# Performance work log

Hardware: AMD Instinct MI355X
Metric: run time of the kernel (lower is better)

Reference implementation:

```python
import jax, jax.numpy as jnp
import numpy as np

B, L, D = 4096, 200, 128


def setup_inputs() -> dict:
    key = jax.random.key(0)
    ks = jax.random.split(key, 9)
    s_in = 1.0 / np.sqrt(2 * D)  # torch Linear default init scale (uniform bound)
    inp = {
        "h_states": jax.random.normal(ks[0], (B, L, D), dtype=jnp.float32),
        "target_emb_proj": jax.random.normal(ks[1], (B, D), dtype=jnp.float32),
        "mask": jax.random.randint(ks[2], (B, L), 0, 2).astype(bool),
        "W_r": jax.random.uniform(ks[3], (2 * D, D), jnp.float32, -s_in, s_in),
        "b_r": jax.random.uniform(ks[4], (D,), jnp.float32, -s_in, s_in),
        "W_u": jax.random.uniform(ks[5], (2 * D, D), jnp.float32, -s_in, s_in),
        "b_u": jax.random.uniform(ks[6], (D,), jnp.float32, -s_in, s_in),
        "W_h": jax.random.uniform(ks[7], (2 * D, D), jnp.float32, -s_in, s_in),
        "b_h": jax.random.uniform(ks[8], (D,), jnp.float32, -s_in, s_in),
    }
    return inp


def reference(h_states, target_emb_proj, mask, W_r, b_r, W_u, b_u, W_h, b_h):
    Bd, Ld, Dd = h_states.shape
    # target-aware attention scores over history: (B, L)
    scores = jnp.einsum("bld,bd->bl", h_states, target_emb_proj) / np.sqrt(Dd).astype(h_states.dtype)
    scores = jnp.where(mask, scores, jnp.asarray(-1e9, scores.dtype))
    attn = jax.nn.softmax(scores, axis=-1)  # (B, L)

    xs = (
        jnp.transpose(h_states, (1, 0, 2)),  # (L, B, D)
        attn.T,                               # (L, B)
        mask.T,                               # (L, B)
    )

    def step(h, x):
        x_t, e_t, m_t = x
        combined = jnp.concatenate([x_t, h], axis=-1)  # (B, 2D)
        r = jax.nn.sigmoid(combined @ W_r + b_r)
        u = jax.nn.sigmoid(combined @ W_u + b_u)
        u_prime = e_t[:, None] * u
        h_tilde = jnp.tanh(jnp.concatenate([x_t, r * h], axis=-1) @ W_h + b_h)
        h_new = (1.0 - u_prime) * h + u_prime * h_tilde
        h_next = jnp.where(m_t[:, None], h_new, h)
        return h_next, None

    h0 = jnp.zeros((Bd, Dd), dtype=h_states.dtype)
    h_final, _ = jax.lax.scan(step, h0, xs)
    return h_final
```

## Files before the change

kernel.cpp:

```cpp
#include <hip/hip_runtime.h>
#include <hip/hip_bf16.h>
#include <stdint.h>

#define LSEQ 200
#define DDIM 128

typedef __attribute__((ext_vector_type(8))) __bf16 bf16x8;
typedef __attribute__((ext_vector_type(4))) float f32x4;

__device__ __forceinline__ float fast_exp(float x) {
  return __builtin_amdgcn_exp2f(x * 1.4426950408889634f);
}
__device__ __forceinline__ float fast_sigmoid(float x) {
  return __builtin_amdgcn_rcpf(1.0f + fast_exp(-x));
}
__device__ __forceinline__ float fast_tanh(float x) {
  float ax = __builtin_fabsf(x);
  float t = __builtin_amdgcn_exp2f(ax * -2.885390081777927f);
  float r = (1.0f - t) * __builtin_amdgcn_rcpf(1.0f + t);
  return x < 0.0f ? -r : r;
}

__device__ __forceinline__ f32x4 mfma16(bf16x8 a, bf16x8 b, f32x4 c) {
  return __builtin_amdgcn_mfma_f32_16x16x32_bf16(a, b, c, 0, 0, 0);
}

__global__ __launch_bounds__(512) void k_scores_pack(
    const float* __restrict__ h_states, const float* __restrict__ target,
    const int* __restrict__ mask, uint4* __restrict__ xp,
    float* __restrict__ attnT, int B) {
  __shared__ float s_sc[4][16][LSEQ];
  __shared__ float s_tgt[16][DDIM];
  const int b16 = blockIdx.x;
  const int bb = b16 * 16;
  const int tid = threadIdx.x;
  for (int i = tid; i < 16 * DDIM; i += 512)
    s_tgt[i >> 7][i & 127] = target[(size_t)(bb + (i >> 7)) * DDIM + (i & 127)];
  __syncthreads();

  const int lane = tid & 63;
  const int kt = (tid >> 6) & 3;
  const int tp = tid >> 8;
  const int row = lane & 15;
  const int hi = lane >> 4;
  const int kbase = kt * 32 + hi * 8;
  const int B16 = B >> 4;
  const float* src = h_states + ((size_t)(bb + row) * LSEQ) * DDIM + kbase;
  const float* tg = &s_tgt[row][kbase];

  for (int t = tp; t < LSEQ; t += 2) {
    float4 a = *(const float4*)(src + (size_t)t * DDIM);
    float4 b = *(const float4*)(src + (size_t)t * DDIM + 4);
    float dv = (a.x * tg[0] + a.y * tg[1] + a.z * tg[2] + a.w * tg[3]) +
               (b.x * tg[4] + b.y * tg[5] + b.z * tg[6] + b.w * tg[7]);
    dv += __shfl_xor(dv, 16);
    dv += __shfl_xor(dv, 32);
    if (hi == 0) s_sc[kt][row][t] = dv;
    union { __bf16 h[8]; uint4 v; } pk;
    pk.h[0] = (__bf16)a.x; pk.h[1] = (__bf16)a.y; pk.h[2] = (__bf16)a.z; pk.h[3] = (__bf16)a.w;
    pk.h[4] = (__bf16)b.x; pk.h[5] = (__bf16)b.y; pk.h[6] = (__bf16)b.z; pk.h[7] = (__bf16)b.w;
    xp[(((size_t)t * B16 + b16) * 4 + kt) * 64 + lane] = pk.v;
  }
  __syncthreads();

  if (tid < 256) {
    const int r2 = tid >> 4;
    const int j = tid & 15;
    const int* mrow = mask + (size_t)(bb + r2) * LSEQ;
    float mx = -3.0e38f;
    for (int t = j; t < LSEQ; t += 16) {
      float s = (s_sc[0][r2][t] + s_sc[1][r2][t]) + (s_sc[2][r2][t] + s_sc[3][r2][t]);
      s *= 0.088388347648318447f;
      s = (mrow[t] != 0) ? s : -3.0e38f;
      s_sc[0][r2][t] = s;
      mx = fmaxf(mx, s);
    }
    mx = fmaxf(mx, __shfl_xor(mx, 1));
    mx = fmaxf(mx, __shfl_xor(mx, 2));
    mx = fmaxf(mx, __shfl_xor(mx, 4));
    mx = fmaxf(mx, __shfl_xor(mx, 8));
    float se = 0.0f;
    for (int t = j; t < LSEQ; t += 16) {
      float e = fast_exp(s_sc[0][r2][t] - mx);
      s_sc[1][r2][t] = e;
      se += e;
    }
    se += __shfl_xor(se, 1);
    se += __shfl_xor(se, 2);
    se += __shfl_xor(se, 4);
    se += __shfl_xor(se, 8);
    float rs = __builtin_amdgcn_rcpf(se);
    for (int t = j; t < LSEQ; t += 16)
      attnT[(size_t)t * B + bb + r2] = (mrow[t] != 0) ? s_sc[1][r2][t] * rs : 0.0f;
  }
}

__global__ __launch_bounds__(512, 2) void k_recur(
    const uint4* __restrict__ xp, const float* __restrict__ attnT,
    const float* __restrict__ Wr, const float* __restrict__ br,
    const float* __restrict__ Wu, const float* __restrict__ bu,
    const float* __restrict__ Wh, const float* __restrict__ bh,
    float* __restrict__ out, int B) {
  __shared__ __bf16 s_rh[16][136];
  __shared__ __bf16 s_hb[16][136];
  __shared__ float s_att[LSEQ][16];
  const int tid = threadIdx.x;
  const int lane = tid & 63;
  const int wv = tid >> 6;
  const int b16 = blockIdx.x;
  const int bb = b16 * 16;
  const int g = lane >> 4;
  const int rA = lane & 15;
  const int col = wv * 16 + rA;
  const int B16 = B >> 4;

  bf16x8 wr[8], wu[8], wh[8];
#pragma unroll
  for (int kt = 0; kt < 8; ++kt) {
    bf16x8 tr, tu, th;
    int krow = kt * 32 + g * 8;
#pragma unroll
    for (int j = 0; j < 8; ++j) {
      tr[j] = (__bf16)Wr[(size_t)(krow + j) * DDIM + col];
      tu[j] = (__bf16)Wu[(size_t)(krow + j) * DDIM + col];
      th[j] = (__bf16)Wh[(size_t)(krow + j) * DDIM + col];
    }
    wr[kt] = tr; wu[kt] = tu; wh[kt] = th;
  }
  const float biasr = br[col], biasu = bu[col], biash = bh[col];

  for (int i = tid; i < LSEQ * 16; i += 512)
    s_att[i >> 4][i & 15] = attnT[(size_t)(i >> 4) * B + bb + (i & 15)];
  for (int i = tid; i < 16 * 136; i += 512)
    (&s_hb[0][0])[i] = (__bf16)0.0f;
  __syncthreads();

  float hD[4] = {0.f, 0.f, 0.f, 0.f};
  uint4 xc[4], xn[4];
  {
    size_t base = (size_t)b16 * 4;
#pragma unroll
    for (int kt = 0; kt < 4; ++kt) xc[kt] = xp[(base + kt) * 64 + lane];
  }

  for (int t = 0; t < LSEQ; ++t) {
    if (t + 1 < LSEQ) {
      size_t base = ((size_t)(t + 1) * B16 + b16) * 4;
#pragma unroll
      for (int kt = 0; kt < 4; ++kt) xn[kt] = xp[(base + kt) * 64 + lane];
    }
    bf16x8 hf[4];
#pragma unroll
    for (int kt = 0; kt < 4; ++kt)
      hf[kt] = *(const bf16x8*)&s_hb[rA][kt * 32 + g * 8];
    f32x4 accr = {biasr, biasr, biasr, biasr};
    f32x4 accu = {biasu, biasu, biasu, biasu};
#pragma unroll
    for (int kt = 0; kt < 4; ++kt) {
      bf16x8 a = __builtin_bit_cast(bf16x8, xc[kt]);
      accr = mfma16(a, wr[kt], accr);
      accu = mfma16(a, wu[kt], accu);
    }
#pragma unroll
    for (int kt = 0; kt < 4; ++kt) {
      accr = mfma16(hf[kt], wr[4 + kt], accr);
      accu = mfma16(hf[kt], wu[4 + kt], accu);
    }
    float rr[4], uu[4];
#pragma unroll
    for (int j = 0; j < 4; ++j) {
      rr[j] = fast_sigmoid(accr[j]);
      uu[j] = fast_sigmoid(accu[j]);
      s_rh[g * 4 + j][col] = (__bf16)(rr[j] * hD[j]);
    }
    __builtin_amdgcn_sched_barrier(0);
    asm volatile("s_waitcnt lgkmcnt(0)" ::: "memory");
    __builtin_amdgcn_s_barrier();
    __builtin_amdgcn_sched_barrier(0);
    bf16x8 rf[4];
#pragma unroll
    for (int kt = 0; kt < 4; ++kt)
      rf[kt] = *(const bf16x8*)&s_rh[rA][kt * 32 + g * 8];
    f32x4 acch = {biash, biash, biash, biash};
#pragma unroll
    for (int kt = 0; kt < 4; ++kt) {
      bf16x8 a = __builtin_bit_cast(bf16x8, xc[kt]);
      acch = mfma16(a, wh[kt], acch);
      acch = mfma16(rf[kt], wh[4 + kt], acch);
    }
#pragma unroll
    for (int j = 0; j < 4; ++j) {
      float ht = fast_tanh(acch[j]);
      float up = s_att[t][g * 4 + j] * uu[j];
      hD[j] += up * (ht - hD[j]);
      s_hb[g * 4 + j][col] = (__bf16)hD[j];
    }
    __builtin_amdgcn_sched_barrier(0);
    asm volatile("s_waitcnt lgkmcnt(0)" ::: "memory");
    __builtin_amdgcn_s_barrier();
    __builtin_amdgcn_sched_barrier(0);
#pragma unroll
    for (int kt = 0; kt < 4; ++kt) xc[kt] = xn[kt];
  }
#pragma unroll
  for (int j = 0; j < 4; ++j)
    out[(size_t)(bb + g * 4 + j) * DDIM + col] = hD[j];
}

extern "C" void kernel_launch(void* const* d_in, const int* in_sizes, int n_in,
                              void* d_out, int out_size, void* d_ws, size_t ws_size,
                              hipStream_t stream) {
  const float* h_states = (const float*)d_in[0];
  const float* target   = (const float*)d_in[1];
  const int*   mask     = (const int*)d_in[2];
  const float* Wr = (const float*)d_in[3];
  const float* br = (const float*)d_in[4];
  const float* Wu = (const float*)d_in[5];
  const float* bu = (const float*)d_in[6];
  const float* Wh = (const float*)d_in[7];
  const float* bh = (const float*)d_in[8];

  const int B = in_sizes[0] / (LSEQ * DDIM);
  uint4* xp = (uint4*)d_ws;
  float* attnT = (float*)((char*)d_ws + (size_t)B * LSEQ * DDIM * 2);

  k_scores_pack<<<B / 16, 512, 0, stream>>>(h_states, target, mask, xp, attnT, B);
  k_recur<<<B / 16, 512, 0, stream>>>(xp, attnT, Wr, br, Wu, bu, Wh, bh,
                                      (float*)d_out, B);
}
```

Before: 316.8 us.

## Fuse score/pack kernel into recurrence and precompute next-step input projections

Merges the scoring/softmax/bf16-pack kernel with the GRU recurrence kernel into one launch per 16-row batch tile. The attention weights now stay in shared memory instead of going through a global buffer, and the packed x layout becomes batch-major so each block reads its own contiguous region. The recurrence is software-pipelined: the x-projection MFMAs for step t+1 are issued during step t, off the h-dependent critical path, with a two-step unrolled loop. This raises shared memory and register use per block, which can reduce occupancy, and it removes the overlap that separate kernels had between the bandwidth-heavy pack phase and compute.

```diff
diff --git a/kernel.cpp b/kernel.cpp
--- a/kernel.cpp
+++ b/kernel.cpp
@@ -25,43 +25,128 @@
   return __builtin_amdgcn_mfma_f32_16x16x32_bf16(a, b, c, 0, 0, 0);
 }
 
-__global__ __launch_bounds__(512) void k_scores_pack(
+#define STEP(t, XC, XN, AXRC, AXUC, AXHC, AXRN, AXUN, AXHN)             \
+  do {                                                                  \
+    if ((t) + 2 < LSEQ) {                                               \
+      size_t pbase = ((size_t)b16 * LSEQ + (t) + 2) * 4;                \
+      _Pragma("unroll") for (int kt = 0; kt < 4; ++kt)                  \
+          XN[kt] = xp[(pbase + kt) * 64 + lane];                        \
+    }                                                                   \
+    bf16x8 hf[4];                                                       \
+    _Pragma("unroll") for (int kt = 0; kt < 4; ++kt)                    \
+        hf[kt] = *(const bf16x8*)&s_hb[rA][kt * 32 + g * 8];            \
+    f32x4 accr = AXRC, accu = AXUC;                                     \
+    if ((t) + 1 < LSEQ) {   \
+      AXRN = (f32x4){biasr, biasr, biasr, biasr};                       \
+      AXUN = (f32x4){biasu, biasu, biasu, biasu};                       \
+      _Pragma("unroll") for (int kt = 0; kt < 4; ++kt) {                \
+        bf16x8 a = __builtin_bit_cast(bf16x8, XC[kt]);                  \
+        AXRN = mfma16(a, wr[kt], AXRN);                                 \
+        AXUN = mfma16(a, wu[kt], AXUN);                                 \
+      }                                                                 \
+    }                                                                   \
+    _Pragma("unroll") for (int kt = 0; kt < 4; ++kt) {                  \
+      accr = mfma16(hf[kt], wr[4 + kt], accr);                          \
+      accu = mfma16(hf[kt], wu[4 + kt], accu);                          \
+    }                                                                   \
+    float rr[4], uu[4];                                                 \
+    _Pragma("unroll") for (int j = 0; j < 4; ++j) {                     \
+      rr[j] = fast_sigmoid(accr[j]);                                    \
+      uu[j] = fast_sigmoid(accu[j]);                                    \
+      s_rh[g * 4 + j][col] = (__bf16)(rr[j] * hD[j]);                   \
+    }                                                                   \
+    __builtin_amdgcn_sched_barrier(0);                                  \
+    asm volatile("s_waitcnt lgkmcnt(0)" ::: "memory");                  \
+    __builtin_amdgcn_s_barrier();                                       \
+    __builtin_amdgcn_sched_barrier(0);                                  \
+    bf16x8 rf[4];                                                       \
+    _Pragma("unroll") for (int kt = 0; kt < 4; ++kt)                    \
+        rf[kt] = *(const bf16x8*)&s_rh[rA][kt * 32 + g * 8];            \
+    f32x4 acch = AXHC;                                                  \
+    if ((t) + 1 < LSEQ) {                                               \
+      AXHN = (f32x4){biash, biash, biash, biash};                       \
+      _Pragma("unroll") for (int kt = 0; kt < 4; ++kt)                  \
+        AXHN = mfma16(__builtin_bit_cast(bf16x8, XC[kt]), wh[kt], AXHN);\
+    }                                                                   \
+    _Pragma("unroll") for (int kt = 0; kt < 4; ++kt)                    \
+      acch = mfma16(rf[kt], wh[4 + kt], acch);                          \
+    _Pragma("unroll") for (int j = 0; j < 4; ++j) {                     \
+      float ht = fast_tanh(acch[j]);                                    \
+      float up = s_att[t][g * 4 + j] * uu[j];                           \
+      hD[j] += up * (ht - hD[j]);                                       \
+      s_hb[g * 4 + j][col] = (__bf16)hD[j];                             \
+    }                                                                   \
+    __builtin_amdgcn_sched_barrier(0);                                  \
+    asm volatile("s_waitcnt lgkmcnt(0)" ::: "memory");                  \
+    __builtin_amdgcn_s_barrier();                                       \
+    __builtin_amdgcn_sched_barrier(0);                                  \
+  } while (0)
+
+__global__ __launch_bounds__(512, 2) void k_fused(
     const float* __restrict__ h_states, const float* __restrict__ target,
-    const int* __restrict__ mask, uint4* __restrict__ xp,
-    float* __restrict__ attnT, int B) {
+    const int* __restrict__ mask,
+    const float* __restrict__ Wr, const float* __restrict__ br,
+    const float* __restrict__ Wu, const float* __restrict__ bu,
+    const float* __restrict__ Wh, const float* __restrict__ bh,
+    uint4* __restrict__ xp, float* __restrict__ out, int B) {
   __shared__ float s_sc[4][16][LSEQ];
   __shared__ float s_tgt[16][DDIM];
+  __shared__ float s_att[LSEQ][16];
+  __shared__ __bf16 s_rh[16][136];
+  __shared__ __bf16 s_hb[16][136];
+
   const int b16 = blockIdx.x;
   const int bb = b16 * 16;
   const int tid = threadIdx.x;
+  const int lane = tid & 63;
+  const int wv = tid >> 6;
+
   for (int i = tid; i < 16 * DDIM; i += 512)
     s_tgt[i >> 7][i & 127] = target[(size_t)(bb + (i >> 7)) * DDIM + (i & 127)];
   __syncthreads();
 
-  const int lane = tid & 63;
-  const int kt = (tid >> 6) & 3;
-  const int tp = tid >> 8;
-  const int row = lane & 15;
-  const int hi = lane >> 4;
-  const int kbase = kt * 32 + hi * 8;
-  const int B16 = B >> 4;
-  const float* src = h_states + ((size_t)(bb + row) * LSEQ) * DDIM + kbase;
-  const float* tg = &s_tgt[row][kbase];
-
-  for (int t = tp; t < LSEQ; t += 2) {
-    float4 a = *(const float4*)(src + (size_t)t * DDIM);
-    float4 b = *(const float4*)(src + (size_t)t * DDIM + 4);
-    float dv = (a.x * tg[0] + a.y * tg[1] + a.z * tg[2] + a.w * tg[3]) +
-               (b.x * tg[4] + b.y * tg[5] + b.z * tg[6] + b.w * tg[7]);
-    dv += __shfl_xor(dv, 16);
-    dv += __shfl_xor(dv, 32);
-    if (hi == 0) s_sc[kt][row][t] = dv;
-    union { __bf16 h[8]; uint4 v; } pk;
-    pk.h[0] = (__bf16)a.x; pk.h[1] = (__bf16)a.y; pk.h[2] = (__bf16)a.z; pk.h[3] = (__bf16)a.w;
-    pk.h[4] = (__bf16)b.x; pk.h[5] = (__bf16)b.y; pk.h[6] = (__bf16)b.z; pk.h[7] = (__bf16)b.w;
-    xp[(((size_t)t * B16 + b16) * 4 + kt) * 64 + lane] = pk.v;
+  {
+    const int kt = (tid >> 6) & 3;
+    const int tp = tid >> 8;
+    const int row = lane & 15;
+    const int hi = lane >> 4;
+    const int kbase = kt * 32 + hi * 8;
+    const float* src = h_states + ((size_t)(bb + row) * LSEQ) * DDIM + kbase;
+    const float* tg = &s_tgt[row][kbase];
+#pragma unroll 2
+    for (int t = tp; t < LSEQ; t += 2) {
+      float4 a = *(const float4*)(src + (size_t)t * DDIM);
+      float4 b = *(const float4*)(src + (size_t)t * DDIM + 4);
+      float dv = (a.x * tg[0] + a.y * tg[1] + a.z * tg[2] + a.w * tg[3]) +
+                 (b.x * tg[4] + b.y * tg[5] + b.z * tg[6] + b.w * tg[7]);
+      dv += __shfl_xor(dv, 16);
+      dv += __shfl_xor(dv, 32);
+      if (hi == 0) s_sc[kt][row][t] = dv;
+      union { __bf16 h[8]; uint4 v; } pk;
+      pk.h[0] = (__bf16)a.x; pk.h[1] = (__bf16)a.y; pk.h[2] = (__bf16)a.z; pk.h[3] = (__bf16)a.w;
+      pk.h[4] = (__bf16)b.x; pk.h[5] = (__bf16)b.y; pk.h[6] = (__bf16)b.z; pk.h[7] = (__bf16)b.w;
+      xp[(((size_t)b16 * LSEQ + t) * 4 + kt) * 64 + lane] = pk.v;
+    }
   }
   __syncthreads();
+
+  const int g = lane >> 4;
+  const int rA = lane & 15;
+  const int col = wv * 16 + rA;
+  bf16x8 wr[8], wu[8], wh[8];
+#pragma unroll
+  for (int kt = 0; kt < 8; ++kt) {
+    bf16x8 tr, tu, th;
+    int krow = kt * 32 + g * 8;
+#pragma unroll
+    for (int j = 0; j < 8; ++j) {
+      tr[j] = (__bf16)Wr[(size_t)(krow + j) * DDIM + col];
+      tu[j] = (__bf16)Wu[(size_t)(krow + j) * DDIM + col];
+      th[j] = (__bf16)Wh[(size_t)(krow + j) * DDIM + col];
+    }
+    wr[kt] = tr; wu[kt] = tu; wh[kt] = th;
+  }
+  const float biasr = br[col], biasu = bu[col], biash = bh[col];
 
   if (tid < 256) {
     const int r2 = tid >> 4;
@@ -91,117 +176,38 @@
     se += __shfl_xor(se, 8);
     float rs = __builtin_amdgcn_rcpf(se);
     for (int t = j; t < LSEQ; t += 16)
-      attnT[(size_t)t * B + bb + r2] = (mrow[t] != 0) ? s_sc[1][r2][t] * rs : 0.0f;
-  }
-}
-
-__global__ __launch_bounds__(512, 2) void k_recur(
-    const uint4* __restrict__ xp, const float* __restrict__ attnT,
-    const float* __restrict__ Wr, const float* __restrict__ br,
-    const float* __restrict__ Wu, const float* __restrict__ bu,
-    const float* __restrict__ Wh, const float* __restrict__ bh,
-    float* __restrict__ out, int B) {
-  __shared__ __bf16 s_rh[16][136];
-  __shared__ __bf16 s_hb[16][136];
-  __shared__ float s_att[LSEQ][16];
-  const int tid = threadIdx.x;
-  const int lane = tid & 63;
-  const int wv = tid >> 6;
-  const int b16 = blockIdx.x;
-  const int bb = b16 * 16;
-  const int g = lane >> 4;
-  const int rA = lane & 15;
-  const int col = wv * 16 + rA;
-  const int B16 = B >> 4;
-
-  bf16x8 wr[8], wu[8], wh[8];
-#pragma unroll
-  for (int kt = 0; kt < 8; ++kt) {
-    bf16x8 tr, tu, th;
-    int krow = kt * 32 + g * 8;
-#pragma unroll
-    for (int j = 0; j < 8; ++j) {
-      tr[j] = (__bf16)Wr[(size_t)(krow + j) * DDIM + col];
-      tu[j] = (__bf16)Wu[(size_t)(krow + j) * DDIM + col];
-      th[j] = (__bf16)Wh[(size_t)(krow + j) * DDIM + col];
-    }
-    wr[kt] = tr; wu[kt] = tu; wh[kt] = th;
-  }
-  const float biasr = br[col], biasu = bu[col], biash = bh[col];
-
-  for (int i = tid; i < LSEQ * 16; i += 512)
-    s_att[i >> 4][i & 15] = attnT[(size_t)(i >> 4) * B + bb + (i & 15)];
+      s_att[t][r2] = (mrow[t] != 0) ? s_sc[1][r2][t] * rs : 0.0f;
+  }
   for (int i = tid; i < 16 * 136; i += 512)
     (&s_hb[0][0])[i] = (__bf16)0.0f;
+
+  uint4 xT[4], xA[4], xB[4];
+  {
+    size_t pbase = (size_t)b16 * LSEQ * 4;
+#pragma unroll
+    for (int kt = 0; kt < 4; ++kt) xT[kt] = xp[(pbase + kt) * 64 + lane];
+#pragma unroll
+    for (int kt = 0; kt < 4; ++kt) xA[kt] = xp[(pbase + 4 + kt) * 64 + lane];
+  }
+  f32x4 axr0 = {biasr, biasr, biasr, biasr};
+  f32x4 axu0 = {biasu, biasu, biasu, biasu};
+  f32x4 axh0 = {biash, biash, biash, biash};
+#pragma unroll
+  for (int kt = 0; kt < 4; ++kt) {
+    bf16x8 a = __builtin_bit_cast(bf16x8, xT[kt]);
+    axr0 = mfma16(a, wr[kt], axr0);
+    axu0 = mfma16(a, wu[kt], axu0);
+    axh0 = mfma16(a, wh[kt], axh0);
+  }
+  f32x4 axr1, axu1, axh1;
+  float hD[4] = {0.f, 0.f, 0.f, 0.f};
   __syncthreads();
 
-  float hD[4] = {0.f, 0.f, 0.f, 0.f};
-  uint4 xc[4], xn[4];
-  {
-    size_t base = (size_t)b16 * 4;
-#pragma unroll
-    for (int kt = 0; kt < 4; ++kt) xc[kt] = xp[(base + kt) * 64 + lane];
-  }
-
-  for (int t = 0; t < LSEQ; ++t) {
-    if (t + 1 < LSEQ) {
-      size_t base = ((size_t)(t + 1) * B16 + b16) * 4;
-#pragma unroll
-      for (int kt = 0; kt < 4; ++kt) xn[kt] = xp[(base + kt) * 64 + lane];
-    }
-    bf16x8 hf[4];
-#pragma unroll
-    for (int kt = 0; kt < 4; ++kt)
-      hf[kt] = *(const bf16x8*)&s_hb[rA][kt * 32 + g * 8];
-    f32x4 accr = {biasr, biasr, biasr, biasr};
-    f32x4 accu = {biasu, biasu, biasu, biasu};
-#pragma unroll
-    for (int kt = 0; kt < 4; ++kt) {
-      bf16x8 a = __builtin_bit_cast(bf16x8, xc[kt]);
-      accr = mfma16(a, wr[kt], accr);
-      accu = mfma16(a, wu[kt], accu);
-    }
-#pragma unroll
-    for (int kt = 0; kt < 4; ++kt) {
-      accr = mfma16(hf[kt], wr[4 + kt], accr);
-      accu = mfma16(hf[kt], wu[4 + kt], accu);
-    }
-    float rr[4], uu[4];
-#pragma unroll
-    for (int j = 0; j < 4; ++j) {
-      rr[j] = fast_sigmoid(accr[j]);
-      uu[j] = fast_sigmoid(accu[j]);
-      s_rh[g * 4 + j][col] = (__bf16)(rr[j] * hD[j]);
-    }
-    __builtin_amdgcn_sched_barrier(0);
-    asm volatile("s_waitcnt lgkmcnt(0)" ::: "memory");
-    __builtin_amdgcn_s_barrier();
-    __builtin_amdgcn_sched_barrier(0);
-    bf16x8 rf[4];
-#pragma unroll
-    for (int kt = 0; kt < 4; ++kt)
-      rf[kt] = *(const bf16x8*)&s_rh[rA][kt * 32 + g * 8];
-    f32x4 acch = {biash, biash, biash, biash};
-#pragma unroll
-    for (int kt = 0; kt < 4; ++kt) {
-      bf16x8 a = __builtin_bit_cast(bf16x8, xc[kt]);
-      acch = mfma16(a, wh[kt], acch);
-      acch = mfma16(rf[kt], wh[4 + kt], acch);
-    }
-#pragma unroll
-    for (int j = 0; j < 4; ++j) {
-      float ht = fast_tanh(acch[j]);
-      float up = s_att[t][g * 4 + j] * uu[j];
-      hD[j] += up * (ht - hD[j]);
-      s_hb[g * 4 + j][col] = (__bf16)hD[j];
-    }
-    __builtin_amdgcn_sched_barrier(0);
-    asm volatile("s_waitcnt lgkmcnt(0)" ::: "memory");
-    __builtin_amdgcn_s_barrier();
-    __builtin_amdgcn_sched_barrier(0);
-#pragma unroll
-    for (int kt = 0; kt < 4; ++kt) xc[kt] = xn[kt];
-  }
+  for (int t = 0; t < LSEQ; t += 2) {
+    STEP(t, xA, xB, axr0, axu0, axh0, axr1, axu1, axh1);
+    STEP(t + 1, xB, xA, axr1, axu1, axh1, axr0, axu0, axh0);
+  }
+
 #pragma unroll
   for (int j = 0; j < 4; ++j)
     out[(size_t)(bb + g * 4 + j) * DDIM + col] = hD[j];
@@ -222,9 +228,7 @@
 
   const int B = in_sizes[0] / (LSEQ * DDIM);
   uint4* xp = (uint4*)d_ws;
-  float* attnT = (float*)((char*)d_ws + (size_t)B * LSEQ * DDIM * 2);
-
-  k_scores_pack<<<B / 16, 512, 0, stream>>>(h_states, target, mask, xp, attnT, B);
-  k_recur<<<B / 16, 512, 0, stream>>>(xp, attnT, Wr, br, Wu, bu, Wh, bh,
-                                      (float*)d_out, B);
-}
+
+  k_fused<<<B / 16, 512, 0, stream>>>(h_states, target, mask, Wr, br, Wu, bu,
+                                      Wh, bh, xp, (float*)d_out, B);
+}
```

Measured after the change: 352.8 us. +11.4%, slower.

## Drop bf16 packed copy, read fp32 inputs in recurrence and precompute next-step x projections

Applied to the files above, without the earlier changes.

The scores kernel no longer writes a bf16 packed copy of h_states. The recurrence kernel now loads fp32 h_states directly, two steps ahead, and converts it in registers. The x-dependent MFMA terms for step t+1 are computed during step t, so they sit off the serial h-dependent chain. The attention buffer is laid out per block so reads are contiguous, and the LDS row pad changes to 138. This removes a large workspace write and read, but doubles the recurrence's global read bytes because inputs are now fp32 and uses more registers.

```diff
diff --git a/kernel.cpp b/kernel.cpp
--- a/kernel.cpp
+++ b/kernel.cpp
@@ -4,6 +4,7 @@
 
 #define LSEQ 200
 #define DDIM 128
+#define PAD 138
 
 typedef __attribute__((ext_vector_type(8))) __bf16 bf16x8;
 typedef __attribute__((ext_vector_type(4))) float f32x4;
@@ -20,15 +21,19 @@
   float r = (1.0f - t) * __builtin_amdgcn_rcpf(1.0f + t);
   return x < 0.0f ? -r : r;
 }
-
 __device__ __forceinline__ f32x4 mfma16(bf16x8 a, bf16x8 b, f32x4 c) {
   return __builtin_amdgcn_mfma_f32_16x16x32_bf16(a, b, c, 0, 0, 0);
 }
-
-__global__ __launch_bounds__(512) void k_scores_pack(
+__device__ __forceinline__ bf16x8 pack8(float4 a, float4 b) {
+  bf16x8 r;
+  r[0] = (__bf16)a.x; r[1] = (__bf16)a.y; r[2] = (__bf16)a.z; r[3] = (__bf16)a.w;
+  r[4] = (__bf16)b.x; r[5] = (__bf16)b.y; r[6] = (__bf16)b.z; r[7] = (__bf16)b.w;
+  return r;
+}
+
+__global__ __launch_bounds__(512) void k_scores(
     const float* __restrict__ h_states, const float* __restrict__ target,
-    const int* __restrict__ mask, uint4* __restrict__ xp,
-    float* __restrict__ attnT, int B) {
+    const int* __restrict__ mask, float* __restrict__ attnT, int B) {
   __shared__ float s_sc[4][16][LSEQ];
   __shared__ float s_tgt[16][DDIM];
   const int b16 = blockIdx.x;
@@ -38,28 +43,25 @@
     s_tgt[i >> 7][i & 127] = target[(size_t)(bb + (i >> 7)) * DDIM + (i & 127)];
   __syncthreads();
 
-  const int lane = tid & 63;
-  const int kt = (tid >> 6) & 3;
-  const int tp = tid >> 8;
-  const int row = lane & 15;
-  const int hi = lane >> 4;
-  const int kbase = kt * 32 + hi * 8;
-  const int B16 = B >> 4;
-  const float* src = h_states + ((size_t)(bb + row) * LSEQ) * DDIM + kbase;
-  const float* tg = &s_tgt[row][kbase];
-
-  for (int t = tp; t < LSEQ; t += 2) {
-    float4 a = *(const float4*)(src + (size_t)t * DDIM);
-    float4 b = *(const float4*)(src + (size_t)t * DDIM + 4);
-    float dv = (a.x * tg[0] + a.y * tg[1] + a.z * tg[2] + a.w * tg[3]) +
-               (b.x * tg[4] + b.y * tg[5] + b.z * tg[6] + b.w * tg[7]);
-    dv += __shfl_xor(dv, 16);
-    dv += __shfl_xor(dv, 32);
-    if (hi == 0) s_sc[kt][row][t] = dv;
-    union { __bf16 h[8]; uint4 v; } pk;
-    pk.h[0] = (__bf16)a.x; pk.h[1] = (__bf16)a.y; pk.h[2] = (__bf16)a.z; pk.h[3] = (__bf16)a.w;
-    pk.h[4] = (__bf16)b.x; pk.h[5] = (__bf16)b.y; pk.h[6] = (__bf16)b.z; pk.h[7] = (__bf16)b.w;
-    xp[(((size_t)t * B16 + b16) * 4 + kt) * 64 + lane] = pk.v;
+  {
+    const int lane = tid & 63;
+    const int kt = (tid >> 6) & 3;
+    const int tp = tid >> 8;
+    const int row = lane & 15;
+    const int hi = lane >> 4;
+    const int kbase = kt * 32 + hi * 8;
+    const float* src = h_states + ((size_t)(bb + row) * LSEQ) * DDIM + kbase;
+    const float* tg = &s_tgt[row][kbase];
+#pragma unroll 2
+    for (int t = tp; t < LSEQ; t += 2) {
+      float4 a = *(const float4*)(src + (size_t)t * DDIM);
+      float4 b = *(const float4*)(src + (size_t)t * DDIM + 4);
+      float dv = (a.x * tg[0] + a.y * tg[1] + a.z * tg[2] + a.w * tg[3]) +
+                 (b.x * tg[4] + b.y * tg[5] + b.z * tg[6] + b.w * tg[7]);
+      dv += __shfl_xor(dv, 16);
+      dv += __shfl_xor(dv, 32);
+      if (hi == 0) s_sc[kt][row][t] = dv;
+    }
   }
   __syncthreads();
 
@@ -91,18 +93,81 @@
     se += __shfl_xor(se, 8);
     float rs = __builtin_amdgcn_rcpf(se);
     for (int t = j; t < LSEQ; t += 16)
-      attnT[(size_t)t * B + bb + r2] = (mrow[t] != 0) ? s_sc[1][r2][t] * rs : 0.0f;
-  }
-}
+      attnT[((size_t)b16 * LSEQ + t) * 16 + r2] =
+          (mrow[t] != 0) ? s_sc[1][r2][t] * rs : 0.0f;
+  }
+}
+
+#define STEP(t, XC, XN, AXRC, AXUC, AXHC, AXRN, AXUN, AXHN)                  \
+  do {                                                                       \
+    if ((t) + 2 < LSEQ) {                                                    \
+      _Pragma("unroll") for (int kt = 0; kt < 4; ++kt) {                     \
+        XN[2 * kt] = *(const float4*)(srcx + (size_t)((t) + 2) * DDIM + kt * 32); \
+        XN[2 * kt + 1] =                                                     \
+            *(const float4*)(srcx + (size_t)((t) + 2) * DDIM + kt * 32 + 4); \
+      }                                                                      \
+    }                                                                        \
+    f32x4 att4 = *(const f32x4*)&s_att[(t)][g * 4];                          \
+    bf16x8 hf[4];                                                            \
+    _Pragma("unroll") for (int kt = 0; kt < 4; ++kt)                         \
+        hf[kt] = *(const bf16x8*)&s_hb[rA][kt * 32 + g * 8];                 \
+    f32x4 accr = AXRC, accu = AXUC;                                          \
+    bf16x8 af[4];                                                            \
+    if ((t) + 1 < LSEQ) {         \
+      _Pragma("unroll") for (int kt = 0; kt < 4; ++kt)                       \
+          af[kt] = pack8(XC[2 * kt], XC[2 * kt + 1]);                        \
+      AXRN = (f32x4){biasr, biasr, biasr, biasr};                            \
+      AXUN = (f32x4){biasu, biasu, biasu, biasu};                            \
+      _Pragma("unroll") for (int kt = 0; kt < 4; ++kt) {                     \
+        AXRN = mfma16(af[kt], wr[kt], AXRN);                                 \
+        AXUN = mfma16(af[kt], wu[kt], AXUN);                                 \
+      }                                                                      \
+    }                                                                        \
+    _Pragma("unroll") for (int kt = 0; kt < 4; ++kt) {                       \
+      accr = mfma16(hf[kt], wr[4 + kt], accr);                               \
+      accu = mfma16(hf[kt], wu[4 + kt], accu);                               \
+    }                                                                        \
+    float rr[4], uu[4];                                                      \
+    _Pragma("unroll") for (int j = 0; j < 4; ++j) {                          \
+      rr[j] = fast_sigmoid(accr[j]);                                         \
+      uu[j] = fast_sigmoid(accu[j]);                                         \
+      s_rh[g * 4 + j][col] = (__bf16)(rr[j] * hD[j]);                        \
+    }                                                                        \
+    __builtin_amdgcn_sched_barrier(0);                                       \
+    asm volatile("s_waitcnt lgkmcnt(0)" ::: "memory");                       \
+    __builtin_amdgcn_s_barrier();                                            \
+    __builtin_amdgcn_sched_barrier(0);                                       \
+    bf16x8 rf[4];                                                            \
+    _Pragma("unroll") for (int kt = 0; kt < 4; ++kt)                         \
+        rf[kt] = *(const bf16x8*)&s_rh[rA][kt * 32 + g * 8];                 \
+    f32x4 acch = AXHC;                                                       \
+    if ((t) + 1 < LSEQ) {                                                    \
+      AXHN = (f32x4){biash, biash, biash, biash};                            \
+      _Pragma("unroll") for (int kt = 0; kt < 4; ++kt)                       \
+          AXHN = mfma16(af[kt], wh[kt], AXHN);                               \
+    }                                                                        \
+    _Pragma("unroll") for (int kt = 0; kt < 4; ++kt)                         \
+        acch = mfma16(rf[kt], wh[4 + kt], acch);                             \
+    _Pragma("unroll") for (int j = 0; j < 4; ++j) {                          \
+      float ht = fast_tanh(acch[j]);                                         \
+      float up = att4[j] * uu[j];                                            \
+      hD[j] += up * (ht - hD[j]);                                            \
+      s_hb[g * 4 + j][col] = (__bf16)hD[j];                                  \
+    }                                                                        \
+    __builtin_amdgcn_sched_barrier(0);                                       \
+    asm volatile("s_waitcnt lgkmcnt(0)" ::: "memory");                       \
+    __builtin_amdgcn_s_barrier();                                            \
+    __builtin_amdgcn_sched_barrier(0);                                       \
+  } while (0)
 
 __global__ __launch_bounds__(512, 2) void k_recur(
-    const uint4* __restrict__ xp, const float* __restrict__ attnT,
+    const float* __restrict__ h_states, const float* __restrict__ attnT,
     const float* __restrict__ Wr, const float* __restrict__ br,
     const float* __restrict__ Wu, const float* __restrict__ bu,
     const float* __restrict__ Wh, const float* __restrict__ bh,
     float* __restrict__ out, int B) {
-  __shared__ __bf16 s_rh[16][136];
-  __shared__ __bf16 s_hb[16][136];
+  __shared__ __bf16 s_rh[16][PAD];
+  __shared__ __bf16 s_hb[16][PAD];
   __shared__ float s_att[LSEQ][16];
   const int tid = threadIdx.x;
   const int lane = tid & 63;
@@ -112,7 +177,6 @@
   const int g = lane >> 4;
   const int rA = lane & 15;
   const int col = wv * 16 + rA;
-  const int B16 = B >> 4;
 
   bf16x8 wr[8], wu[8], wh[8];
 #pragma unroll
@@ -130,78 +194,42 @@
   const float biasr = br[col], biasu = bu[col], biash = bh[col];
 
   for (int i = tid; i < LSEQ * 16; i += 512)
-    s_att[i >> 4][i & 15] = attnT[(size_t)(i >> 4) * B + bb + (i & 15)];
-  for (int i = tid; i < 16 * 136; i += 512)
+    s_att[i >> 4][i & 15] = attnT[(size_t)b16 * LSEQ * 16 + i];
+  for (int i = tid; i < 16 * PAD; i += 512)
     (&s_hb[0][0])[i] = (__bf16)0.0f;
+
+  const float* srcx = h_states + ((size_t)(bb + rA) * LSEQ) * DDIM + g * 8;
+
+  float4 xA[8], xB[8];
+#pragma unroll
+  for (int kt = 0; kt < 4; ++kt) {
+    xB[2 * kt] = *(const float4*)(srcx + kt * 32);
+    xB[2 * kt + 1] = *(const float4*)(srcx + kt * 32 + 4);
+  }
+  f32x4 axr0 = {biasr, biasr, biasr, biasr};
+  f32x4 axu0 = {biasu, biasu, biasu, biasu};
+  f32x4 axh0 = {biash, biash, biash, biash};
+#pragma unroll
+  for (int kt = 0; kt < 4; ++kt) {
+    bf16x8 a = pack8(xB[2 * kt], xB[2 * kt + 1]);
+    axr0 = mfma16(a, wr[kt], axr0);
+    axu0 = mfma16(a, wu[kt], axu0);
+    axh0 = mfma16(a, wh[kt], axh0);
+  }
+#pragma unroll
+  for (int kt = 0; kt < 4; ++kt) {
+    xA[2 * kt] = *(const float4*)(srcx + DDIM + kt * 32);
+    xA[2 * kt + 1] = *(const float4*)(srcx + DDIM + kt * 32 + 4);
+  }
+  f32x4 axr1, axu1, axh1;
+  float hD[4] = {0.f, 0.f, 0.f, 0.f};
   __syncthreads();
 
-  float hD[4] = {0.f, 0.f, 0.f, 0.f};
-  uint4 xc[4], xn[4];
-  {
-    size_t base = (size_t)b16 * 4;
-#pragma unroll
-    for (int kt = 0; kt < 4; ++kt) xc[kt] = xp[(base + kt) * 64 + lane];
-  }
-
-  for (int t = 0; t < LSEQ; ++t) {
-    if (t + 1 < LSEQ) {
-      size_t base = ((size_t)(t + 1) * B16 + b16) * 4;
-#pragma unroll
-      for (int kt = 0; kt < 4; ++kt) xn[kt] = xp[(base + kt) * 64 + lane];
-    }
-    bf16x8 hf[4];
-#pragma unroll
-    for (int kt = 0; kt < 4; ++kt)
-      hf[kt] = *(const bf16x8*)&s_hb[rA][kt * 32 + g * 8];
-    f32x4 accr = {biasr, biasr, biasr, biasr};
-    f32x4 accu = {biasu, biasu, biasu, biasu};
-#pragma unroll
-    for (int kt = 0; kt < 4; ++kt) {
-      bf16x8 a = __builtin_bit_cast(bf16x8, xc[kt]);
-      accr = mfma16(a, wr[kt], accr);
-      accu = mfma16(a, wu[kt], accu);
-    }
-#pragma unroll
-    for (int kt = 0; kt < 4; ++kt) {
-      accr = mfma16(hf[kt], wr[4 + kt], accr);
-      accu = mfma16(hf[kt], wu[4 + kt], accu);
-    }
-    float rr[4], uu[4];
-#pragma unroll
-    for (int j = 0; j < 4; ++j) {
-      rr[j] = fast_sigmoid(accr[j]);
-      uu[j] = fast_sigmoid(accu[j]);
-      s_rh[g * 4 + j][col] = (__bf16)(rr[j] * hD[j]);
-    }
-    __builtin_amdgcn_sched_barrier(0);
-    asm volatile("s_waitcnt lgkmcnt(0)" ::: "memory");
-    __builtin_amdgcn_s_barrier();
-    __builtin_amdgcn_sched_barrier(0);
-    bf16x8 rf[4];
-#pragma unroll
-    for (int kt = 0; kt < 4; ++kt)
-      rf[kt] = *(const bf16x8*)&s_rh[rA][kt * 32 + g * 8];
-    f32x4 acch = {biash, biash, biash, biash};
-#pragma unroll
-    for (int kt = 0; kt < 4; ++kt) {
-      bf16x8 a = __builtin_bit_cast(bf16x8, xc[kt]);
-      acch = mfma16(a, wh[kt], acch);
-      acch = mfma16(rf[kt], wh[4 + kt], acch);
-    }
-#pragma unroll
-    for (int j = 0; j < 4; ++j) {
-      float ht = fast_tanh(acch[j]);
-      float up = s_att[t][g * 4 + j] * uu[j];
-      hD[j] += up * (ht - hD[j]);
-      s_hb[g * 4 + j][col] = (__bf16)hD[j];
-    }
-    __builtin_amdgcn_sched_barrier(0);
-    asm volatile("s_waitcnt lgkmcnt(0)" ::: "memory");
-    __builtin_amdgcn_s_barrier();
-    __builtin_amdgcn_sched_barrier(0);
-#pragma unroll
-    for (int kt = 0; kt < 4; ++kt) xc[kt] = xn[kt];
-  }
+  for (int t = 0; t < LSEQ; t += 2) {
+    STEP(t, xA, xB, axr0, axu0, axh0, axr1, axu1, axh1);
+    STEP(t + 1, xB, xA, axr1, axu1, axh1, axr0, axu0, axh0);
+  }
+
 #pragma unroll
   for (int j = 0; j < 4; ++j)
     out[(size_t)(bb + g * 4 + j) * DDIM + col] = hD[j];
@@ -221,10 +249,9 @@
   const float* bh = (const float*)d_in[8];
 
   const int B = in_sizes[0] / (LSEQ * DDIM);
-  uint4* xp = (uint4*)d_ws;
-  float* attnT = (float*)((char*)d_ws + (size_t)B * LSEQ * DDIM * 2);
-
-  k_scores_pack<<<B / 16, 512, 0, stream>>>(h_states, target, mask, xp, attnT, B);
-  k_recur<<<B / 16, 512, 0, stream>>>(xp, attnT, Wr, br, Wu, bu, Wh, bh,
+  float* attnT = (float*)d_ws;
+
+  k_scores<<<B / 16, 512, 0, stream>>>(h_states, target, mask, attnT, B);
+  k_recur<<<B / 16, 512, 0, stream>>>(h_states, attnT, Wr, br, Wu, bu, Wh, bh,
                                       (float*)d_out, B);
 }
```

Result: slower. 696.5 us (+119.9%).
